# Optimization experiments

Hardware: AMD Instinct MI355X
Metric: run time of the kernel (lower is better)

Reference implementation:

```python
import jax, jax.numpy as jnp
import numpy as np

B, S, D, H, G = 16, 512, 1024, 128, 256  # batch, seq, lstm_in, lstm_hidden, gat_dim

def _linear(x, W, b):
    return x @ W.T + b

def _lstm_dir(xs, Wih, Whh, bih, bhh, reverse):
    # xs: [S, B, Din] -> hs: [S, B, H]; PyTorch gate order i, f, g, o
    b = bih + bhh
    def step(carry, xt):
        h, c = carry
        z = xt @ Wih.T + h @ Whh.T + b
        i, f, g, o = jnp.split(z, 4, axis=-1)
        c = jax.nn.sigmoid(f) * c + jax.nn.sigmoid(i) * jnp.tanh(g)
        h = jax.nn.sigmoid(o) * jnp.tanh(c)
        return (h, c), h
    init = (jnp.zeros((xs.shape[1], Whh.shape[1]), xs.dtype),
            jnp.zeros((xs.shape[1], Whh.shape[1]), xs.dtype))
    _, hs = jax.lax.scan(step, init, xs, reverse=reverse)
    return hs

def _forward(x, adj,
             l0f_Wih, l0f_Whh, l0f_bih, l0f_bhh, l0b_Wih, l0b_Whh, l0b_bih, l0b_bhh,
             l1f_Wih, l1f_Whh, l1f_bih, l1f_bhh, l1b_Wih, l1b_Whh, l1b_bih, l1b_bhh,
             fc1_W, fc1_b, wattn_W, wattn_b, lin0_W, lin0_b, lin1_W, lin1_b,
             linf_W, linf_b, fcA_W, fcA_b, fcB_W, fcB_b, fcC_W, fcC_b):
    # ---- 2-layer bidirectional LSTM ----
    xs = jnp.swapaxes(x, 0, 1)  # [S, B, D]
    h0 = jnp.concatenate([_lstm_dir(xs, l0f_Wih, l0f_Whh, l0f_bih, l0f_bhh, False),
                          _lstm_dir(xs, l0b_Wih, l0b_Whh, l0b_bih, l0b_bhh, True)], axis=-1)
    h1 = jnp.concatenate([_lstm_dir(h0, l1f_Wih, l1f_Whh, l1f_bih, l1f_bhh, False),
                          _lstm_dir(h0, l1b_Wih, l1b_Whh, l1b_bih, l1b_bhh, True)], axis=-1)
    out_lstm = jnp.swapaxes(h1, 0, 1)  # [B, S, 2H]
    # ---- GAT on fc1(x) ----
    g = _linear(x, fc1_W, fc1_b)  # [B, S, G]
    idx = jnp.arange(S)
    adj = adj.at[:, idx, idx].set(1.0)
    eye = 1e-05 * jnp.eye(S, dtype=x.dtype)
    for l in range(4):
        g0 = g
        q = _linear(g, wattn_W[l], wattn_b[l])
        a = jax.nn.sigmoid(jnp.einsum('bij,bkj->bik', q, g)) + eye
        a = a * adj
        a = a / jnp.sum(a, axis=2, keepdims=True)
        g = jnp.einsum('bij,bjd->bid', a, g)
        g = jax.nn.relu(_linear(g, lin0_W[l], lin0_b[l]))
        g = jax.nn.relu(_linear(g, lin1_W[l], lin1_b[l]))
        g = g + g0
    g = _linear(g, linf_W, linf_b)
    # ---- head (dropout in eval mode -> identity) ----
    hidden = jnp.mean(jnp.concatenate([out_lstm, g], axis=2), axis=1)  # [B, 512]
    y = jax.nn.leaky_relu(_linear(hidden, fcA_W, fcA_b), 0.1)
    y = jax.nn.leaky_relu(_linear(y, fcB_W, fcB_b), 0.1)
    y = _linear(y, fcC_W, fcC_b)  # [B, 2]
    return y, hidden


def setup_inputs() -> dict:
    key = jax.random.key(0)
    ks = jax.random.split(key, 40)
    r = lambda k, shape: jax.random.normal(k, shape, jnp.float32) * 0.05
    inp = {}
    inp['x'] = jax.random.normal(ks[0], (B, S, D), jnp.float32)
    inp['adj'] = (jax.random.uniform(ks[1], (B, S, S)) < 0.05).astype(jnp.float32)
    # LSTM params: layer0 input D, layer1 input 2H; forward/backward directions
    inp['l0f_Wih'] = r(ks[2], (4 * H, D)); inp['l0f_Whh'] = r(ks[3], (4 * H, H))
    inp['l0f_bih'] = r(ks[4], (4 * H,));  inp['l0f_bhh'] = r(ks[5], (4 * H,))
    inp['l0b_Wih'] = r(ks[6], (4 * H, D)); inp['l0b_Whh'] = r(ks[7], (4 * H, H))
    inp['l0b_bih'] = r(ks[8], (4 * H,));  inp['l0b_bhh'] = r(ks[9], (4 * H,))
    inp['l1f_Wih'] = r(ks[10], (4 * H, 2 * H)); inp['l1f_Whh'] = r(ks[11], (4 * H, H))
    inp['l1f_bih'] = r(ks[12], (4 * H,)); inp['l1f_bhh'] = r(ks[13], (4 * H,))
    inp['l1b_Wih'] = r(ks[14], (4 * H, 2 * H)); inp['l1b_Whh'] = r(ks[15], (4 * H, H))
    inp['l1b_bih'] = r(ks[16], (4 * H,)); inp['l1b_bhh'] = r(ks[17], (4 * H,))
    inp['fc1_W'] = r(ks[18], (G, D)); inp['fc1_b'] = r(ks[19], (G,))
    inp['wattn_W'] = r(ks[20], (4, G, G)); inp['wattn_b'] = r(ks[21], (4, G))
    inp['lin0_W'] = r(ks[22], (4, G, G)); inp['lin0_b'] = r(ks[23], (4, G))
    inp['lin1_W'] = r(ks[24], (4, G, G)); inp['lin1_b'] = r(ks[25], (4, G))
    inp['linf_W'] = r(ks[26], (G, G)); inp['linf_b'] = r(ks[27], (G,))
    inp['fcA_W'] = r(ks[28], (128, 512)); inp['fcA_b'] = r(ks[29], (128,))
    inp['fcB_W'] = r(ks[30], (32, 128)); inp['fcB_b'] = r(ks[31], (32,))
    inp['fcC_W'] = r(ks[32], (2, 32)); inp['fcC_b'] = r(ks[33], (2,))
    return inp


def reference(x, adj,
              l0f_Wih, l0f_Whh, l0f_bih, l0f_bhh, l0b_Wih, l0b_Whh, l0b_bih, l0b_bhh,
              l1f_Wih, l1f_Whh, l1f_bih, l1f_bhh, l1b_Wih, l1b_Whh, l1b_bih, l1b_bhh,
              fc1_W, fc1_b, wattn_W, wattn_b, lin0_W, lin0_b, lin1_W, lin1_b,
              linf_W, linf_b, fcA_W, fcA_b, fcB_W, fcB_b, fcC_W, fcC_b):
    return _forward(x, adj,
                    l0f_Wih, l0f_Whh, l0f_bih, l0f_bhh, l0b_Wih, l0b_Whh, l0b_bih, l0b_bhh,
                    l1f_Wih, l1f_Whh, l1f_bih, l1f_bhh, l1b_Wih, l1b_Whh, l1b_bih, l1b_bhh,
                    fc1_W, fc1_b, wattn_W, wattn_b, lin0_W, lin0_b, lin1_W, lin1_b,
                    linf_W, linf_b, fcA_W, fcA_b, fcB_W, fcB_b, fcC_W, fcC_b)
```

## Files before the change

### kernel.cpp

```cpp
#include <hip/hip_runtime.h>
#include <stdint.h>

#define B_ 16
#define S_ 512
#define D_ 1024
#define H4 512
#define G_ 256

typedef unsigned short u16;
using short8 = __attribute__((ext_vector_type(8))) short;
using f32x4  = __attribute__((ext_vector_type(4))) float;

__device__ __forceinline__ u16 f2bf(float f){
  unsigned int u = __float_as_uint(f);
  u += 0x7fffu + ((u >> 16) & 1u);
  return (u16)(u >> 16);
}
__device__ __forceinline__ float bf2f(u16 h){
  return __uint_as_float(((unsigned int)h) << 16);
}

struct CvtSegs {
  const float4* src[14];
  short4* dst[14];
  int blk0[15];
};
__global__ __launch_bounds__(256) void cvt_multi(CvtSegs cs){
  int blk = blockIdx.x;
  int s = 0;
  #pragma unroll
  for (int k = 0; k < 14; ++k) if (cs.blk0[k + 1] <= blk) s = k + 1;
  int i = (blk - cs.blk0[s]) * 256 + threadIdx.x;
  float4 v = cs.src[s][i];
  short4 o;
  o.x = (short)f2bf(v.x); o.y = (short)f2bf(v.y);
  o.z = (short)f2bf(v.z); o.w = (short)f2bf(v.w);
  cs.dst[s][i] = o;
}

__global__ __launch_bounds__(256) void bias_prep(const float* a,const float* b,const float* c,const float* d,
                                                 const float* e,const float* f,const float* g,const float* h,
                                                 float* out){
  int i = blockIdx.x * 256 + threadIdx.x;
  if (i >= 2048) return;
  int p = i >> 9, k = i & 511;
  const float* x1 = (p==0)?a:(p==1)?c:(p==2)?e:g;
  const float* x2 = (p==0)?b:(p==1)?d:(p==2)?f:h;
  out[i] = x1[k] + x2[k];
}

template<int ACT, bool OUT_BF16, int PERM, bool RESID>
__device__ __forceinline__ void gemm_bt_body(
    const u16* __restrict__ A, const u16* __restrict__ W,
    const float* __restrict__ bias, const u16* __restrict__ resid,
    void* __restrict__ outp, int M, int N, int K,
    long sA, long sW, long sO, int bx, int by, int bz)
{
  const u16* Ab = A + (long)bz * sA;
  const u16* Wb = W + (long)bz * sW;
  const int bm0 = by * 64, bn0 = bx * 64;
  const int tid = threadIdx.x;
  const int l = tid & 63, wid = tid >> 6;
  const int wm = (wid >> 1) * 32, wn = (wid & 1) * 32;
  const int lr = l & 15, lk8 = (l >> 4) * 8;

  const f32x4 z4 = {0.f, 0.f, 0.f, 0.f};
  f32x4 acc[2][2] = {{z4, z4}, {z4, z4}};

  const u16* Ap0 = Ab + (long)(bm0 + wm + lr) * K + lk8;
  const u16* Wp0 = Wb + (long)(bn0 + wn + lr) * K + lk8;
  for (int k0 = 0; k0 < K; k0 += 32) {
    short8 a0 = *reinterpret_cast<const short8*>(Ap0 + k0);
    short8 a1 = *reinterpret_cast<const short8*>(Ap0 + (long)16 * K + k0);
    short8 b0 = *reinterpret_cast<const short8*>(Wp0 + k0);
    short8 b1 = *reinterpret_cast<const short8*>(Wp0 + (long)16 * K + k0);
    acc[0][0] = __builtin_amdgcn_mfma_f32_16x16x32_bf16(a0, b0, acc[0][0], 0, 0, 0);
    acc[0][1] = __builtin_amdgcn_mfma_f32_16x16x32_bf16(a0, b1, acc[0][1], 0, 0, 0);
    acc[1][0] = __builtin_amdgcn_mfma_f32_16x16x32_bf16(a1, b0, acc[1][0], 0, 0, 0);
    acc[1][1] = __builtin_amdgcn_mfma_f32_16x16x32_bf16(a1, b1, acc[1][1], 0, 0, 0);
  }
  #pragma unroll
  for (int mt = 0; mt < 2; ++mt)
  #pragma unroll
  for (int nt = 0; nt < 2; ++nt) {
    int n = bn0 + wn + 16 * nt + lr;
    float bv = bias ? bias[n] : 0.f;
    #pragma unroll
    for (int r = 0; r < 4; ++r) {
      int m = bm0 + wm + 16 * mt + (l >> 4) * 4 + r;
      float v = acc[mt][nt][r] + bv;
      if (ACT == 1) v = fmaxf(v, 0.f);
      if (RESID) v += bf2f(resid[(long)m * N + n]);
      long oi;
      if (PERM == 2) {
        int t = m & 511, b = m >> 9;
        oi = (long)((t * 16 + b) * 128 + (n & 127)) * 4 + (n >> 7);
      } else {
        oi = (long)bz * sO + (long)m * N + n;
      }
      if (OUT_BF16) ((u16*)outp)[oi] = f2bf(v);
      else          ((float*)outp)[oi] = v;
    }
  }
}

template<int ACT, bool OUT_BF16, int PERM, bool RESID>
__global__ __launch_bounds__(256) void gemm_bt(
    const u16* __restrict__ A, const u16* __restrict__ W,
    const float* __restrict__ bias, const u16* __restrict__ resid,
    void* __restrict__ outp, int M, int N, int K,
    long sA, long sW, long sO)
{
  gemm_bt_body<ACT, OUT_BF16, PERM, RESID>(A, W, bias, resid, outp, M, N, K,
                                           sA, sW, sO, blockIdx.x, blockIdx.y, blockIdx.z);
}

__device__ __forceinline__ void lstm_scan_body(
    const float* __restrict__ X, const u16* __restrict__ Whh,
    u16* __restrict__ Hout, int dir, int bg)
{
  __shared__ __align__(16) u16 h_lds[16 * 136];
  __shared__ float z_lds[4 * 516];

  const int tid = threadIdx.x;
  const int l = tid & 63, w = tid >> 6;
  const int lr = l & 15, lk = l >> 4;

  short8 bfrag[4][4];
  #pragma unroll
  for (int nt = 0; nt < 4; ++nt)
    #pragma unroll
    for (int ks = 0; ks < 4; ++ks)
      bfrag[nt][ks] = *reinterpret_cast<const short8*>(
          Whh + (64 * w + 16 * nt + lr) * 128 + 32 * ks + 8 * lk);

  for (int i = tid; i < 16 * 136; i += 512) h_lds[i] = 0;

  const int j  = tid & 127;
  const int bq = tid >> 7;
  float c = 0.f;
  const f32x4 z4 = {0.f, 0.f, 0.f, 0.f};

  __syncthreads();

  auto ldX = [&](int t) -> float4 {
    int ta = dir ? (S_ - 1 - t) : t;
    return *reinterpret_cast<const float4*>(X + (long)((ta * 16 + bg + bq) * 128 + j) * 4);
  };

  float4 x0 = ldX(0), x1 = ldX(1), x2 = ldX(2), x3;

  auto step = [&](int t, float4& xc, float4& xt, int tload) {
    short8 af[4];
    #pragma unroll
    for (int ks = 0; ks < 4; ++ks)
      af[ks] = *reinterpret_cast<const short8*>(h_lds + lr * 136 + 32 * ks + 8 * lk);
    f32x4 acc[4] = {z4, z4, z4, z4};
    #pragma unroll
    for (int nt = 0; nt < 4; ++nt)
      #pragma unroll
      for (int ks = 0; ks < 4; ++ks)
        acc[nt] = __builtin_amdgcn_mfma_f32_16x16x32_bf16(af[ks], bfrag[nt][ks], acc[nt], 0, 0, 0);
    if (lk == 0) {
      #pragma unroll
      for (int nt = 0; nt < 4; ++nt)
        #pragma unroll
        for (int r = 0; r < 4; ++r)
          z_lds[r * 516 + 64 * w + 16 * nt + lr] = acc[nt][r];
    }
    if (tload < S_) xt = ldX(tload);
    asm volatile("s_waitcnt lgkmcnt(0)" ::: "memory");
    __builtin_amdgcn_s_barrier();
    int ta = dir ? (S_ - 1 - t) : t;
    float zi = z_lds[bq * 516 + j      ] + xc.x;
    float zf = z_lds[bq * 516 + 128 + j] + xc.y;
    float zg = z_lds[bq * 516 + 256 + j] + xc.z;
    float zo = z_lds[bq * 516 + 384 + j] + xc.w;
    float si = __fdividef(1.f, 1.f + __expf(-zi));
    float sf = __fdividef(1.f, 1.f + __expf(-zf));
    float so = __fdividef(1.f, 1.f + __expf(-zo));
    float eg = __expf(2.f * zg);
    float tg = 1.f - __fdividef(2.f, eg + 1.f);
    c = sf * c + si * tg;
    float ec = __expf(2.f * c);
    float tc = 1.f - __fdividef(2.f, ec + 1.f);
    float hv = so * tc;
    u16 hb = f2bf(hv);
    h_lds[bq * 136 + j] = hb;
    Hout[((long)(bg + bq) * S_ + ta) * 256 + dir * 128 + j] = hb;
    asm volatile("s_waitcnt lgkmcnt(0)" ::: "memory");
    __builtin_amdgcn_s_barrier();
  };

  for (int t = 0; t < S_; t += 4) {
    step(t,     x0, x3, t + 3);
    step(t + 1, x1, x0, t + 4);
    step(t + 2, x2, x1, t + 5);
    step(t + 3, x3, x2, t + 6);
  }
}

__global__ __launch_bounds__(512, 1) void scan_fused(
    const float* __restrict__ Xf, const float* __restrict__ Xb,
    const u16* __restrict__ Whhf, const u16* __restrict__ Whhb,
    u16* __restrict__ Hout,
    const u16* __restrict__ gA, const u16* __restrict__ gW,
    const float* __restrict__ gb, u16* __restrict__ gOut, int gK)
{
  if (blockIdx.x < 8) {
    int dir = blockIdx.x & 1, bg = (blockIdx.x >> 1) * 4;
    lstm_scan_body(dir ? Xb : Xf, dir ? Whhb : Whhf, Hout, dir, bg);
  } else if (threadIdx.x < 256) {
    int bi = blockIdx.x - 8;
    gemm_bt_body<0, true, 0, false>(gA, gW, gb, nullptr, gOut,
                                    8192, 256, gK, 0, 0, 0, bi & 3, bi >> 2, 0);
  }
}

__global__ __launch_bounds__(256) void attn_norm(
    const float* __restrict__ sc, const float* __restrict__ adj, u16* __restrict__ abf)
{
  int bz = blockIdx.y;
  int i = blockIdx.x * 4 + (threadIdx.x >> 6);
  int l = threadIdx.x & 63;
  const float* srow = sc  + ((long)bz * 512 + i) * 512;
  const float* arow = adj + ((long)bz * 512 + i) * 512;
  float av[8]; float sum = 0.f;
  #pragma unroll
  for (int k = 0; k < 8; ++k) {
    int jj = l + 64 * k;
    float sg = __fdividef(1.f, 1.f + __expf(-srow[jj]));
    float v = (jj == i) ? (sg + 1e-5f) : sg * arow[jj];
    av[k] = v; sum += v;
  }
  #pragma unroll
  for (int off = 32; off; off >>= 1) sum += __shfl_xor(sum, off);
  float r = __fdividef(1.f, sum);
  u16* orow = abf + ((long)bz * 512 + i) * 512;
  #pragma unroll
  for (int k = 0; k < 8; ++k) orow[l + 64 * k] = f2bf(av[k] * r);
}

__global__ __launch_bounds__(256) void transpose_g(const u16* __restrict__ in, u16* __restrict__ out)
{
  __shared__ u16 tile[32][33];
  int bz = blockIdx.z;
  int s0 = blockIdx.x * 32, d0 = blockIdx.y * 32;
  int tx = threadIdx.x & 31, ty = threadIdx.x >> 5;
  const u16* ip = in + (long)bz * 512 * 256;
  u16* op = out + (long)bz * 256 * 512;
  #pragma unroll
  for (int k = 0; k < 32; k += 8) tile[ty + k][tx] = ip[(long)(s0 + ty + k) * 256 + d0 + tx];
  __syncthreads();
  #pragma unroll
  for (int k = 0; k < 32; k += 8) op[(long)(d0 + ty + k) * 512 + s0 + tx] = tile[tx][ty + k];
}

__global__ __launch_bounds__(256) void mean_cat(
    const u16* __restrict__ lstm, const u16* __restrict__ gf, float* __restrict__ dout)
{
  int b = blockIdx.x;
  for (int cc = threadIdx.x; cc < 512; cc += 256) {
    const u16* src = (cc < 256) ? (lstm + (long)b * 512 * 256 + cc)
                                : (gf   + (long)b * 512 * 256 + (cc - 256));
    float s = 0.f;
    for (int t = 0; t < 512; ++t) s += bf2f(src[(long)t * 256]);
    dout[32 + b * 512 + cc] = s * (1.f / 512.f);
  }
}

__global__ __launch_bounds__(256) void head_kernel(
    const float* __restrict__ hidden,
    const float* __restrict__ fcA_W, const float* __restrict__ fcA_b,
    const float* __restrict__ fcB_W, const float* __restrict__ fcB_b,
    const float* __restrict__ fcC_W, const float* __restrict__ fcC_b,
    float* __restrict__ y)
{
  __shared__ float hb[16 * 512];
  __shared__ float ab[16 * 128];
  __shared__ float bb[16 * 32];
  int tid = threadIdx.x;
  for (int i = tid; i < 8192; i += 256) hb[i] = hidden[i];
  __syncthreads();
  for (int o = tid; o < 2048; o += 256) {
    int b = o >> 7, jj = o & 127;
    float acc = fcA_b[jj];
    const float* wrow = fcA_W + jj * 512;
    const float* hrow = hb + b * 512;
    for (int k = 0; k < 512; ++k) acc += hrow[k] * wrow[k];
    ab[o] = acc > 0.f ? acc : 0.1f * acc;
  }
  __syncthreads();
  for (int o = tid; o < 512; o += 256) {
    int b = o >> 5, jj = o & 31;
    float acc = fcB_b[jj];
    for (int k = 0; k < 128; ++k) acc += ab[b * 128 + k] * fcB_W[jj * 128 + k];
    bb[o] = acc > 0.f ? acc : 0.1f * acc;
  }
  __syncthreads();
  if (tid < 32) {
    int b = tid >> 1, jj = tid & 1;
    float acc = fcC_b[jj];
    for (int k = 0; k < 32; ++k) acc += bb[b * 32 + k] * fcC_W[jj * 32 + k];
    y[b * 2 + jj] = acc;
  }
}

extern "C" void kernel_launch(void* const* d_in, const int* in_sizes, int n_in,
                              void* d_out, int out_size, void* d_ws, size_t ws_size,
                              hipStream_t stream)
{
  const float* x       = (const float*)d_in[0];
  const float* adj     = (const float*)d_in[1];
  const float* l0f_Wih = (const float*)d_in[2];
  const float* l0f_Whh = (const float*)d_in[3];
  const float* l0f_bih = (const float*)d_in[4];
  const float* l0f_bhh = (const float*)d_in[5];
  const float* l0b_Wih = (const float*)d_in[6];
  const float* l0b_Whh = (const float*)d_in[7];
  const float* l0b_bih = (const float*)d_in[8];
  const float* l0b_bhh = (const float*)d_in[9];
  const float* l1f_Wih = (const float*)d_in[10];
  const float* l1f_Whh = (const float*)d_in[11];
  const float* l1f_bih = (const float*)d_in[12];
  const float* l1f_bhh = (const float*)d_in[13];
  const float* l1b_Wih = (const float*)d_in[14];
  const float* l1b_Whh = (const float*)d_in[15];
  const float* l1b_bih = (const float*)d_in[16];
  const float* l1b_bhh = (const float*)d_in[17];
  const float* fc1_W   = (const float*)d_in[18];
  const float* fc1_b   = (const float*)d_in[19];
  const float* wattn_W = (const float*)d_in[20];
  const float* wattn_b = (const float*)d_in[21];
  const float* lin0_W  = (const float*)d_in[22];
  const float* lin0_b  = (const float*)d_in[23];
  const float* lin1_W  = (const float*)d_in[24];
  const float* lin1_b  = (const float*)d_in[25];
  const float* linf_W  = (const float*)d_in[26];
  const float* linf_b  = (const float*)d_in[27];
  const float* fcA_W   = (const float*)d_in[28];
  const float* fcA_b   = (const float*)d_in[29];
  const float* fcB_W   = (const float*)d_in[30];
  const float* fcB_b   = (const float*)d_in[31];
  const float* fcC_W   = (const float*)d_in[32];
  const float* fcC_b   = (const float*)d_in[33];

  char* wp = (char*)d_ws;
  auto alloc = [&](size_t n) -> void* { void* p = wp; wp += (n + 255) & ~(size_t)255; return p; };

  u16* x_bf     = (u16*)alloc((size_t)B_ * S_ * D_ * 2);
  u16* w0f_ih   = (u16*)alloc((size_t)512 * 1024 * 2);
  u16* w0f_hh   = (u16*)alloc((size_t)512 * 128 * 2);
  u16* w0b_ih   = (u16*)alloc((size_t)512 * 1024 * 2);
  u16* w0b_hh   = (u16*)alloc((size_t)512 * 128 * 2);
  u16* w1f_ih   = (u16*)alloc((size_t)512 * 256 * 2);
  u16* w1f_hh   = (u16*)alloc((size_t)512 * 128 * 2);
  u16* w1b_ih   = (u16*)alloc((size_t)512 * 256 * 2);
  u16* w1b_hh   = (u16*)alloc((size_t)512 * 128 * 2);
  u16* wfc1     = (u16*)alloc((size_t)256 * 1024 * 2);
  u16* wattn_bf = (u16*)alloc((size_t)4 * 256 * 256 * 2);
  u16* wlin0_bf = (u16*)alloc((size_t)4 * 256 * 256 * 2);
  u16* wlin1_bf = (u16*)alloc((size_t)4 * 256 * 256 * 2);
  u16* wlinf_bf = (u16*)alloc((size_t)256 * 256 * 2);
  float* bias4  = (float*)alloc((size_t)2048 * 4);
  float* X0f    = (float*)alloc((size_t)S_ * 16 * 512 * 4);
  float* X0b    = (float*)alloc((size_t)S_ * 16 * 512 * 4);
  u16* h0       = (u16*)alloc((size_t)B_ * S_ * 256 * 2);
  u16* lstm_out = (u16*)alloc((size_t)B_ * S_ * 256 * 2);
  u16* gA       = (u16*)alloc((size_t)B_ * S_ * 256 * 2);
  u16* gB       = (u16*)alloc((size_t)B_ * S_ * 256 * 2);
  u16* qb       = (u16*)alloc((size_t)B_ * S_ * 256 * 2);
  u16* gT       = (u16*)alloc((size_t)B_ * S_ * 256 * 2);
  u16* t1       = (u16*)alloc((size_t)B_ * S_ * 256 * 2);
  u16* t2       = (u16*)alloc((size_t)B_ * S_ * 256 * 2);
  float* sc     = (float*)alloc((size_t)B_ * S_ * S_ * 4);
  u16* abf      = (u16*)alloc((size_t)B_ * S_ * S_ * 2);

  CvtSegs cs;
  int nb = 0, si = 0;
  auto seg = [&](const float* s, u16* d, int n) {
    cs.src[si] = (const float4*)s; cs.dst[si] = (short4*)d;
    cs.blk0[si] = nb; nb += (n / 4 + 255) / 256; ++si;
  };
  seg(x, x_bf, B_ * S_ * D_);
  seg(l0f_Wih, w0f_ih, 512 * 1024); seg(l0f_Whh, w0f_hh, 512 * 128);
  seg(l0b_Wih, w0b_ih, 512 * 1024); seg(l0b_Whh, w0b_hh, 512 * 128);
  seg(l1f_Wih, w1f_ih, 512 * 256);  seg(l1f_Whh, w1f_hh, 512 * 128);
  seg(l1b_Wih, w1b_ih, 512 * 256);  seg(l1b_Whh, w1b_hh, 512 * 128);
  seg(fc1_W, wfc1, 256 * 1024);
  seg(wattn_W, wattn_bf, 4 * 256 * 256);
  seg(lin0_W, wlin0_bf, 4 * 256 * 256);
  seg(lin1_W, wlin1_bf, 4 * 256 * 256);
  seg(linf_W, wlinf_bf, 256 * 256);
  cs.blk0[si] = nb;
  cvt_multi<<<nb, 256, 0, stream>>>(cs);
  bias_prep<<<8, 256, 0, stream>>>(l0f_bih, l0f_bhh, l0b_bih, l0b_bhh,
                                   l1f_bih, l1f_bhh, l1b_bih, l1b_bhh, bias4);

  gemm_bt<0, false, 2, false><<<dim3(8, 128, 1), 256, 0, stream>>>(
      x_bf, w0f_ih, bias4 + 0, nullptr, X0f, 8192, 512, 1024, 0, 0, 0);
  gemm_bt<0, false, 2, false><<<dim3(8, 128, 1), 256, 0, stream>>>(
      x_bf, w0b_ih, bias4 + 512, nullptr, X0b, 8192, 512, 1024, 0, 0, 0);
  scan_fused<<<8 + 512, 512, 0, stream>>>(X0f, X0b, w0f_hh, w0b_hh, h0,
                                          x_bf, wfc1, fc1_b, gA, 1024);
  gemm_bt<0, false, 2, false><<<dim3(8, 128, 1), 256, 0, stream>>>(
      h0, w1f_ih, bias4 + 1024, nullptr, X0f, 8192, 512, 256, 0, 0, 0);
  gemm_bt<0, false, 2, false><<<dim3(8, 128, 1), 256, 0, stream>>>(
      h0, w1b_ih, bias4 + 1536, nullptr, X0b, 8192, 512, 256, 0, 0, 0);
  scan_fused<<<8 + 512, 512, 0, stream>>>(X0f, X0b, w1f_hh, w1b_hh, lstm_out,
                                          gA, wattn_bf, wattn_b, qb, 256);

  u16* gcur = gA; u16* gnext = gB;
  for (int lyr = 0; lyr < 4; ++lyr) {
    if (lyr > 0)
      gemm_bt<0, true, 0, false><<<dim3(4, 128, 1), 256, 0, stream>>>(
          gcur, wattn_bf + lyr * 65536, wattn_b + lyr * 256, nullptr, qb, 8192, 256, 256, 0, 0, 0);
    gemm_bt<0, false, 0, false><<<dim3(8, 8, 16), 256, 0, stream>>>(
        qb, gcur, nullptr, nullptr, sc, 512, 512, 256, 131072, 131072, 262144);
    attn_norm<<<dim3(128, 16), 256, 0, stream>>>(sc, adj, abf);
    transpose_g<<<dim3(16, 8, 16), 256, 0, stream>>>(gcur, gT);
    gemm_bt<0, true, 0, false><<<dim3(4, 8, 16), 256, 0, stream>>>(
        abf, gT, nullptr, nullptr, t1, 512, 256, 512, 262144, 131072, 131072);
    gemm_bt<1, true, 0, false><<<dim3(4, 128, 1), 256, 0, stream>>>(
        t1, wlin0_bf + lyr * 65536, lin0_b + lyr * 256, nullptr, t2, 8192, 256, 256, 0, 0, 0);
    gemm_bt<1, true, 0, true><<<dim3(4, 128, 1), 256, 0, stream>>>(
        t2, wlin1_bf + lyr * 65536, lin1_b + lyr * 256, gcur, gnext, 8192, 256, 256, 0, 0, 0);
    u16* tmp = gcur; gcur = gnext; gnext = tmp;
  }
  gemm_bt<0, true, 0, false><<<dim3(4, 128, 1), 256, 0, stream>>>(
      gcur, wlinf_bf, linf_b, nullptr, t2, 8192, 256, 256, 0, 0, 0);

  mean_cat<<<16, 256, 0, stream>>>(lstm_out, t2, (float*)d_out);
  head_kernel<<<1, 256, 0, stream>>>((const float*)d_out + 32,
                                     fcA_W, fcA_b, fcB_W, fcB_b, fcC_W, fcC_b,
                                     (float*)d_out);
}
```

Before: 1.506 ms.

## Interleave two batch chains per LSTM scan block with gate-interleaved weights

The LSTM recurrence now runs 4 blocks instead of 8, and each block advances two independent 4-batch chains. The chains are interleaved so one chain's MFMA work overlaps the other's gate math. W_hh rows are permuted into gate-interleaved order and the MFMA operands are swapped, so each lane gets its i,f,g,o pre-activations for one unit as a single vector. A double-buffered h buffer lets each timestep end with one barrier instead of two. In exchange, each block does twice the serial work per step, and fewer blocks run the scan.

```diff
diff --git a/kernel.cpp b/kernel.cpp
--- a/kernel.cpp
+++ b/kernel.cpp
@@ -36,6 +36,21 @@
   o.x = (short)f2bf(v.x); o.y = (short)f2bf(v.y);
   o.z = (short)f2bf(v.z); o.w = (short)f2bf(v.w);
   cs.dst[s][i] = o;
+}
+
+__global__ __launch_bounds__(256) void cvt_whh(const float* m0, const float* m1,
+                                               const float* m2, const float* m3,
+                                               u16* out){
+  int e = blockIdx.x * 256 + threadIdx.x;
+  int row = e >> 4;
+  int kk = (e & 15) * 8;
+  int mat = row >> 9, c = row & 511;
+  const float* src = (mat == 0 ? m0 : mat == 1 ? m1 : mat == 2 ? m2 : m3)
+                     + ((c & 3) * 128 + (c >> 2)) * 128 + kk;
+  u16* dst = out + (size_t)row * 128 + kk;
+  float4 v0 = *(const float4*)src, v1 = *(const float4*)(src + 4);
+  dst[0] = f2bf(v0.x); dst[1] = f2bf(v0.y); dst[2] = f2bf(v0.z); dst[3] = f2bf(v0.w);
+  dst[4] = f2bf(v1.x); dst[5] = f2bf(v1.y); dst[6] = f2bf(v1.z); dst[7] = f2bf(v1.w);
 }
 
 __global__ __launch_bounds__(256) void bias_prep(const float* a,const float* b,const float* c,const float* d,
@@ -115,103 +130,109 @@
                                            sA, sW, sO, blockIdx.x, blockIdx.y, blockIdx.z);
 }
 
-__device__ __forceinline__ void lstm_scan_body(
-    const float* __restrict__ X, const u16* __restrict__ Whh,
-    u16* __restrict__ Hout, int dir, int bg)
-{
-  __shared__ __align__(16) u16 h_lds[16 * 136];
-  __shared__ float z_lds[4 * 516];
+__device__ __forceinline__ void lstm_scan2_body(
+    const float* __restrict__ X, const u16* __restrict__ Wp,
+    u16* __restrict__ Hout, int dir, int batA, int batB)
+{
+  __shared__ __align__(16) u16 hbuf[2][2][16][4][8];
+  __shared__ __align__(16) float zq[2][8][16][4][4];
 
   const int tid = threadIdx.x;
   const int l = tid & 63, w = tid >> 6;
   const int lr = l & 15, lk = l >> 4;
-
-  short8 bfrag[4][4];
+  const int j = 16 * w + lr;
+
+  short8 wfrag[4][4];
   #pragma unroll
   for (int nt = 0; nt < 4; ++nt)
     #pragma unroll
     for (int ks = 0; ks < 4; ++ks)
-      bfrag[nt][ks] = *reinterpret_cast<const short8*>(
-          Whh + (64 * w + 16 * nt + lr) * 128 + 32 * ks + 8 * lk);
-
-  for (int i = tid; i < 16 * 136; i += 512) h_lds[i] = 0;
-
-  const int j  = tid & 127;
-  const int bq = tid >> 7;
-  float c = 0.f;
+      wfrag[nt][ks] = *reinterpret_cast<const short8*>(
+          Wp + (64 * w + 16 * nt + lr) * 128 + 32 * ks + 8 * lk);
+
+  for (int i = tid; i < (int)(sizeof(hbuf) / 2); i += 512) ((u16*)hbuf)[i] = 0;
+
+  float cA = 0.f, cB = 0.f;
+
+  auto ldX = [&](int bat, int t) -> float4 {
+    int ta = dir ? (S_ - 1 - t) : t;
+    return *reinterpret_cast<const float4*>(X + (size_t)((ta * 16 + bat + lk) * 128 + j) * 4);
+  };
+
+  float4 a0 = ldX(batA, 0), a1 = ldX(batA, 1), a2 = ldX(batA, 2), a3;
+  float4 b0 = ldX(batB, 0), b1 = ldX(batB, 1), b2 = ldX(batB, 2), b3;
+
+  __syncthreads();
+
   const f32x4 z4 = {0.f, 0.f, 0.f, 0.f};
 
-  __syncthreads();
-
-  auto ldX = [&](int t) -> float4 {
-    int ta = dir ? (S_ - 1 - t) : t;
-    return *reinterpret_cast<const float4*>(X + (long)((ta * 16 + bg + bq) * 128 + j) * 4);
-  };
-
-  float4 x0 = ldX(0), x1 = ldX(1), x2 = ldX(2), x3;
-
-  auto step = [&](int t, float4& xc, float4& xt, int tload) {
-    short8 af[4];
+  auto mfma_half = [&](int ch, int p) {
+    short8 hf[4];
     #pragma unroll
     for (int ks = 0; ks < 4; ++ks)
-      af[ks] = *reinterpret_cast<const short8*>(h_lds + lr * 136 + 32 * ks + 8 * lk);
+      hf[ks] = *reinterpret_cast<const short8*>(&hbuf[ch][p][lk + 4 * ks][lr & 3][0]);
     f32x4 acc[4] = {z4, z4, z4, z4};
     #pragma unroll
     for (int nt = 0; nt < 4; ++nt)
       #pragma unroll
       for (int ks = 0; ks < 4; ++ks)
-        acc[nt] = __builtin_amdgcn_mfma_f32_16x16x32_bf16(af[ks], bfrag[nt][ks], acc[nt], 0, 0, 0);
-    if (lk == 0) {
+        acc[nt] = __builtin_amdgcn_mfma_f32_16x16x32_bf16(wfrag[nt][ks], hf[ks], acc[nt], 0, 0, 0);
+    if (lr < 4) {
       #pragma unroll
       for (int nt = 0; nt < 4; ++nt)
-        #pragma unroll
-        for (int r = 0; r < 4; ++r)
-          z_lds[r * 516 + 64 * w + 16 * nt + lr] = acc[nt][r];
+        *reinterpret_cast<f32x4*>(&zq[ch][w][4 * nt + lk][lr][0]) = acc[nt];
     }
-    if (tload < S_) xt = ldX(tload);
-    asm volatile("s_waitcnt lgkmcnt(0)" ::: "memory");
-    __builtin_amdgcn_s_barrier();
-    int ta = dir ? (S_ - 1 - t) : t;
-    float zi = z_lds[bq * 516 + j      ] + xc.x;
-    float zf = z_lds[bq * 516 + 128 + j] + xc.y;
-    float zg = z_lds[bq * 516 + 256 + j] + xc.z;
-    float zo = z_lds[bq * 516 + 384 + j] + xc.w;
+  };
+
+  auto gates = [&](int ch, float& cs, const float4& xc, int bat, int t, int p) {
+    f32x4 q = *reinterpret_cast<const f32x4*>(&zq[ch][w][lr][lk][0]);
+    float zi = q[0] + xc.x, zf = q[1] + xc.y, zg = q[2] + xc.z, zo = q[3] + xc.w;
     float si = __fdividef(1.f, 1.f + __expf(-zi));
     float sf = __fdividef(1.f, 1.f + __expf(-zf));
     float so = __fdividef(1.f, 1.f + __expf(-zo));
     float eg = __expf(2.f * zg);
     float tg = 1.f - __fdividef(2.f, eg + 1.f);
-    c = sf * c + si * tg;
-    float ec = __expf(2.f * c);
+    cs = sf * cs + si * tg;
+    float ec = __expf(2.f * cs);
     float tc = 1.f - __fdividef(2.f, ec + 1.f);
     float hv = so * tc;
     u16 hb = f2bf(hv);
-    h_lds[bq * 136 + j] = hb;
-    Hout[((long)(bg + bq) * S_ + ta) * 256 + dir * 128 + j] = hb;
+    hbuf[ch][p ^ 1][j >> 3][lk][j & 7] = hb;
+    int ta = dir ? (S_ - 1 - t) : t;
+    Hout[((size_t)(bat + lk) * S_ + ta) * 256 + dir * 128 + j] = hb;
+  };
+
+  auto period = [&](int t, float4& xA, float4& xB, float4& pA, float4& pB, int tload) {
+    const int p = t & 1;
+    mfma_half(0, p);
+    mfma_half(1, p);
+    gates(0, cA, xA, batA, t, p);
+    gates(1, cB, xB, batB, t, p);
+    if (tload < S_) { pA = ldX(batA, tload); pB = ldX(batB, tload); }
     asm volatile("s_waitcnt lgkmcnt(0)" ::: "memory");
     __builtin_amdgcn_s_barrier();
   };
 
   for (int t = 0; t < S_; t += 4) {
-    step(t,     x0, x3, t + 3);
-    step(t + 1, x1, x0, t + 4);
-    step(t + 2, x2, x1, t + 5);
-    step(t + 3, x3, x2, t + 6);
+    period(t,     a0, b0, a3, b3, t + 3);
+    period(t + 1, a1, b1, a0, b0, t + 4);
+    period(t + 2, a2, b2, a1, b1, t + 5);
+    period(t + 3, a3, b3, a2, b2, t + 6);
   }
 }
 
 __global__ __launch_bounds__(512, 1) void scan_fused(
     const float* __restrict__ Xf, const float* __restrict__ Xb,
-    const u16* __restrict__ Whhf, const u16* __restrict__ Whhb,
+    const u16* __restrict__ WpF, const u16* __restrict__ WpB,
     u16* __restrict__ Hout,
     const u16* __restrict__ gA, const u16* __restrict__ gW,
     const float* __restrict__ gb, u16* __restrict__ gOut, int gK)
 {
-  if (blockIdx.x < 8) {
-    int dir = blockIdx.x & 1, bg = (blockIdx.x >> 1) * 4;
-    lstm_scan_body(dir ? Xb : Xf, dir ? Whhb : Whhf, Hout, dir, bg);
+  if (blockIdx.x < 4) {
+    int dir = blockIdx.x >> 1, pr = blockIdx.x & 1;
+    lstm_scan2_body(dir ? Xb : Xf, dir ? WpB : WpF, Hout, dir, pr * 8, pr * 8 + 4);
   } else if (threadIdx.x < 256) {
-    int bi = blockIdx.x - 8;
+    int bi = blockIdx.x - 4;
     gemm_bt_body<0, true, 0, false>(gA, gW, gb, nullptr, gOut,
                                     8192, 256, gK, 0, 0, 0, bi & 3, bi >> 2, 0);
   }
@@ -350,13 +371,10 @@
 
   u16* x_bf     = (u16*)alloc((size_t)B_ * S_ * D_ * 2);
   u16* w0f_ih   = (u16*)alloc((size_t)512 * 1024 * 2);
-  u16* w0f_hh   = (u16*)alloc((size_t)512 * 128 * 2);
   u16* w0b_ih   = (u16*)alloc((size_t)512 * 1024 * 2);
-  u16* w0b_hh   = (u16*)alloc((size_t)512 * 128 * 2);
   u16* w1f_ih   = (u16*)alloc((size_t)512 * 256 * 2);
-  u16* w1f_hh   = (u16*)alloc((size_t)512 * 128 * 2);
   u16* w1b_ih   = (u16*)alloc((size_t)512 * 256 * 2);
-  u16* w1b_hh   = (u16*)alloc((size_t)512 * 128 * 2);
+  u16* wI       = (u16*)alloc((size_t)4 * 512 * 128 * 2);
   u16* wfc1     = (u16*)alloc((size_t)256 * 1024 * 2);
   u16* wattn_bf = (u16*)alloc((size_t)4 * 256 * 256 * 2);
   u16* wlin0_bf = (u16*)alloc((size_t)4 * 256 * 256 * 2);
@@ -383,17 +401,18 @@
     cs.blk0[si] = nb; nb += (n / 4 + 255) / 256; ++si;
   };
   seg(x, x_bf, B_ * S_ * D_);
-  seg(l0f_Wih, w0f_ih, 512 * 1024); seg(l0f_Whh, w0f_hh, 512 * 128);
-  seg(l0b_Wih, w0b_ih, 512 * 1024); seg(l0b_Whh, w0b_hh, 512 * 128);
-  seg(l1f_Wih, w1f_ih, 512 * 256);  seg(l1f_Whh, w1f_hh, 512 * 128);
-  seg(l1b_Wih, w1b_ih, 512 * 256);  seg(l1b_Whh, w1b_hh, 512 * 128);
+  seg(l0f_Wih, w0f_ih, 512 * 1024);
+  seg(l0b_Wih, w0b_ih, 512 * 1024);
+  seg(l1f_Wih, w1f_ih, 512 * 256);
+  seg(l1b_Wih, w1b_ih, 512 * 256);
   seg(fc1_W, wfc1, 256 * 1024);
   seg(wattn_W, wattn_bf, 4 * 256 * 256);
   seg(lin0_W, wlin0_bf, 4 * 256 * 256);
   seg(lin1_W, wlin1_bf, 4 * 256 * 256);
   seg(linf_W, wlinf_bf, 256 * 256);
-  cs.blk0[si] = nb;
+  for (int k = si; k <= 14; ++k) cs.blk0[k] = nb;
   cvt_multi<<<nb, 256, 0, stream>>>(cs);
+  cvt_whh<<<128, 256, 0, stream>>>(l0f_Whh, l0b_Whh, l1f_Whh, l1b_Whh, wI);
   bias_prep<<<8, 256, 0, stream>>>(l0f_bih, l0f_bhh, l0b_bih, l0b_bhh,
                                    l1f_bih, l1f_bhh, l1b_bih, l1b_bhh, bias4);
 
@@ -401,13 +420,13 @@
       x_bf, w0f_ih, bias4 + 0, nullptr, X0f, 8192, 512, 1024, 0, 0, 0);
   gemm_bt<0, false, 2, false><<<dim3(8, 128, 1), 256, 0, stream>>>(
       x_bf, w0b_ih, bias4 + 512, nullptr, X0b, 8192, 512, 1024, 0, 0, 0);
-  scan_fused<<<8 + 512, 512, 0, stream>>>(X0f, X0b, w0f_hh, w0b_hh, h0,
+  scan_fused<<<4 + 512, 512, 0, stream>>>(X0f, X0b, wI + 0 * 65536, wI + 1 * 65536, h0,
                                           x_bf, wfc1, fc1_b, gA, 1024);
   gemm_bt<0, false, 2, false><<<dim3(8, 128, 1), 256, 0, stream>>>(
       h0, w1f_ih, bias4 + 1024, nullptr, X0f, 8192, 512, 256, 0, 0, 0);
   gemm_bt<0, false, 2, false><<<dim3(8, 128, 1), 256, 0, stream>>>(
       h0, w1b_ih, bias4 + 1536, nullptr, X0b, 8192, 512, 256, 0, 0, 0);
-  scan_fused<<<8 + 512, 512, 0, stream>>>(X0f, X0b, w1f_hh, w1b_hh, lstm_out,
+  scan_fused<<<4 + 512, 512, 0, stream>>>(X0f, X0b, wI + 2 * 65536, wI + 3 * 65536, lstm_out,
                                           gA, wattn_bf, wattn_b, qb, 256);
 
   u16* gcur = gA; u16* gnext = gB;
```

Result: slower. 2.102 ms (+39.6%).

## Split LSTM scan into 16 blocks of two batches and use direct-load side GEMM

Applied to the files above, without the earlier changes.

The recurrent scan now runs on 16 workgroups, each handling two batch rows instead of four, which halves the per-step gate work and the z_lds traffic per block. MFMA work per step is unchanged because the 16-row tile is padded, so only the half of threads with bq<2 compute gates. The side GEMM fused into the same launch is replaced by a simpler 64x128 tile kernel that loads operands straight from global memory without LDS staging, and it uses all 512 threads across 256 blocks. Weight conversion segments are reordered, which has no speed intent. The trade-off is twice as many serial-latency scan blocks and a GEMM with less data reuse.

```diff
diff --git a/kernel.cpp b/kernel.cpp
--- a/kernel.cpp
+++ b/kernel.cpp
@@ -115,12 +115,52 @@
                                            sA, sW, sO, blockIdx.x, blockIdx.y, blockIdx.z);
 }
 
-__device__ __forceinline__ void lstm_scan_body(
+__device__ __forceinline__ void gemm_bt_body8(
+    const u16* __restrict__ A, const u16* __restrict__ W,
+    const float* __restrict__ bias, u16* __restrict__ out,
+    int N, int K, int bx, int by)
+{
+  const int bm0 = by * 64, bn0 = bx * 128;
+  const int tid = threadIdx.x;
+  const int l = tid & 63, wid = tid >> 6;
+  const int wm = (wid >> 2) * 32, wn = (wid & 3) * 32;
+  const int lr = l & 15, lk8 = (l >> 4) * 8;
+
+  const f32x4 z4 = {0.f, 0.f, 0.f, 0.f};
+  f32x4 acc[2][2] = {{z4, z4}, {z4, z4}};
+
+  const u16* Ap0 = A + (long)(bm0 + wm + lr) * K + lk8;
+  const u16* Wp0 = W + (long)(bn0 + wn + lr) * K + lk8;
+  for (int k0 = 0; k0 < K; k0 += 32) {
+    short8 a0 = *reinterpret_cast<const short8*>(Ap0 + k0);
+    short8 a1 = *reinterpret_cast<const short8*>(Ap0 + (long)16 * K + k0);
+    short8 b0 = *reinterpret_cast<const short8*>(Wp0 + k0);
+    short8 b1 = *reinterpret_cast<const short8*>(Wp0 + (long)16 * K + k0);
+    acc[0][0] = __builtin_amdgcn_mfma_f32_16x16x32_bf16(a0, b0, acc[0][0], 0, 0, 0);
+    acc[0][1] = __builtin_amdgcn_mfma_f32_16x16x32_bf16(a0, b1, acc[0][1], 0, 0, 0);
+    acc[1][0] = __builtin_amdgcn_mfma_f32_16x16x32_bf16(a1, b0, acc[1][0], 0, 0, 0);
+    acc[1][1] = __builtin_amdgcn_mfma_f32_16x16x32_bf16(a1, b1, acc[1][1], 0, 0, 0);
+  }
+  #pragma unroll
+  for (int mt = 0; mt < 2; ++mt)
+  #pragma unroll
+  for (int nt = 0; nt < 2; ++nt) {
+    int n = bn0 + wn + 16 * nt + lr;
+    float bv = bias[n];
+    #pragma unroll
+    for (int r = 0; r < 4; ++r) {
+      int m = bm0 + wm + 16 * mt + (l >> 4) * 4 + r;
+      out[(long)m * N + n] = f2bf(acc[mt][nt][r] + bv);
+    }
+  }
+}
+
+__device__ __forceinline__ void lstm_scan7_body(
     const float* __restrict__ X, const u16* __restrict__ Whh,
     u16* __restrict__ Hout, int dir, int bg)
 {
   __shared__ __align__(16) u16 h_lds[16 * 136];
-  __shared__ float z_lds[4 * 516];
+  __shared__ float z_lds[2 * 516];
 
   const int tid = threadIdx.x;
   const int l = tid & 63, w = tid >> 6;
@@ -139,16 +179,17 @@
   const int j  = tid & 127;
   const int bq = tid >> 7;
   float c = 0.f;
+  float4 xA, xB, xC, xD;
+
+  __syncthreads();
+
+  auto loadX = [&](int t) -> float4 {
+    int ta = dir ? (S_ - 1 - t) : t;
+    return *reinterpret_cast<const float4*>(X + (size_t)((ta * 16 + bg + bq) * 128 + j) * 4);
+  };
+  if (bq < 2) { xA = loadX(0); xB = loadX(1); xC = loadX(2); }
+
   const f32x4 z4 = {0.f, 0.f, 0.f, 0.f};
-
-  __syncthreads();
-
-  auto ldX = [&](int t) -> float4 {
-    int ta = dir ? (S_ - 1 - t) : t;
-    return *reinterpret_cast<const float4*>(X + (long)((ta * 16 + bg + bq) * 128 + j) * 4);
-  };
-
-  float4 x0 = ldX(0), x1 = ldX(1), x2 = ldX(2), x3;
 
   auto step = [&](int t, float4& xc, float4& xt, int tload) {
     short8 af[4];
@@ -165,38 +206,40 @@
       #pragma unroll
       for (int nt = 0; nt < 4; ++nt)
         #pragma unroll
-        for (int r = 0; r < 4; ++r)
+        for (int r = 0; r < 2; ++r)
           z_lds[r * 516 + 64 * w + 16 * nt + lr] = acc[nt][r];
     }
-    if (tload < S_) xt = ldX(tload);
+    if (bq < 2 && tload < S_) xt = loadX(tload);
     asm volatile("s_waitcnt lgkmcnt(0)" ::: "memory");
     __builtin_amdgcn_s_barrier();
-    int ta = dir ? (S_ - 1 - t) : t;
-    float zi = z_lds[bq * 516 + j      ] + xc.x;
-    float zf = z_lds[bq * 516 + 128 + j] + xc.y;
-    float zg = z_lds[bq * 516 + 256 + j] + xc.z;
-    float zo = z_lds[bq * 516 + 384 + j] + xc.w;
-    float si = __fdividef(1.f, 1.f + __expf(-zi));
-    float sf = __fdividef(1.f, 1.f + __expf(-zf));
-    float so = __fdividef(1.f, 1.f + __expf(-zo));
-    float eg = __expf(2.f * zg);
-    float tg = 1.f - __fdividef(2.f, eg + 1.f);
-    c = sf * c + si * tg;
-    float ec = __expf(2.f * c);
-    float tc = 1.f - __fdividef(2.f, ec + 1.f);
-    float hv = so * tc;
-    u16 hb = f2bf(hv);
-    h_lds[bq * 136 + j] = hb;
-    Hout[((long)(bg + bq) * S_ + ta) * 256 + dir * 128 + j] = hb;
+    if (bq < 2) {
+      int ta = dir ? (S_ - 1 - t) : t;
+      float zi = z_lds[bq * 516 + j      ] + xc.x;
+      float zf = z_lds[bq * 516 + 128 + j] + xc.y;
+      float zg = z_lds[bq * 516 + 256 + j] + xc.z;
+      float zo = z_lds[bq * 516 + 384 + j] + xc.w;
+      float si = __fdividef(1.f, 1.f + __expf(-zi));
+      float sf = __fdividef(1.f, 1.f + __expf(-zf));
+      float so = __fdividef(1.f, 1.f + __expf(-zo));
+      float eg = __expf(2.f * zg);
+      float tg = 1.f - __fdividef(2.f, eg + 1.f);
+      c = sf * c + si * tg;
+      float ec = __expf(2.f * c);
+      float tc = 1.f - __fdividef(2.f, ec + 1.f);
+      float hv = so * tc;
+      u16 hb = f2bf(hv);
+      h_lds[bq * 136 + j] = hb;
+      Hout[((size_t)(bg + bq) * S_ + ta) * 256 + dir * 128 + j] = hb;
+    }
     asm volatile("s_waitcnt lgkmcnt(0)" ::: "memory");
     __builtin_amdgcn_s_barrier();
   };
 
   for (int t = 0; t < S_; t += 4) {
-    step(t,     x0, x3, t + 3);
-    step(t + 1, x1, x0, t + 4);
-    step(t + 2, x2, x1, t + 5);
-    step(t + 3, x3, x2, t + 6);
+    step(t,     xA, xD, t + 3);
+    step(t + 1, xB, xA, t + 4);
+    step(t + 2, xC, xB, t + 5);
+    step(t + 3, xD, xC, t + 6);
   }
 }
 
@@ -207,13 +250,12 @@
     const u16* __restrict__ gA, const u16* __restrict__ gW,
     const float* __restrict__ gb, u16* __restrict__ gOut, int gK)
 {
-  if (blockIdx.x < 8) {
-    int dir = blockIdx.x & 1, bg = (blockIdx.x >> 1) * 4;
-    lstm_scan_body(dir ? Xb : Xf, dir ? Whhb : Whhf, Hout, dir, bg);
-  } else if (threadIdx.x < 256) {
-    int bi = blockIdx.x - 8;
-    gemm_bt_body<0, true, 0, false>(gA, gW, gb, nullptr, gOut,
-                                    8192, 256, gK, 0, 0, 0, bi & 3, bi >> 2, 0);
+  if (blockIdx.x < 16) {
+    int dir = blockIdx.x & 1, bg = (blockIdx.x >> 1) * 2;
+    lstm_scan7_body(dir ? Xb : Xf, dir ? Whhb : Whhf, Hout, dir, bg);
+  } else {
+    int bi = blockIdx.x - 16;
+    gemm_bt_body8(gA, gW, gb, gOut, 256, gK, bi & 1, bi >> 1);
   }
 }
 
@@ -350,12 +392,12 @@
 
   u16* x_bf     = (u16*)alloc((size_t)B_ * S_ * D_ * 2);
   u16* w0f_ih   = (u16*)alloc((size_t)512 * 1024 * 2);
+  u16* w0b_ih   = (u16*)alloc((size_t)512 * 1024 * 2);
+  u16* w1f_ih   = (u16*)alloc((size_t)512 * 256 * 2);
+  u16* w1b_ih   = (u16*)alloc((size_t)512 * 256 * 2);
   u16* w0f_hh   = (u16*)alloc((size_t)512 * 128 * 2);
-  u16* w0b_ih   = (u16*)alloc((size_t)512 * 1024 * 2);
   u16* w0b_hh   = (u16*)alloc((size_t)512 * 128 * 2);
-  u16* w1f_ih   = (u16*)alloc((size_t)512 * 256 * 2);
   u16* w1f_hh   = (u16*)alloc((size_t)512 * 128 * 2);
-  u16* w1b_ih   = (u16*)alloc((size_t)512 * 256 * 2);
   u16* w1b_hh   = (u16*)alloc((size_t)512 * 128 * 2);
   u16* wfc1     = (u16*)alloc((size_t)256 * 1024 * 2);
   u16* wattn_bf = (u16*)alloc((size_t)4 * 256 * 256 * 2);
@@ -383,16 +425,20 @@
     cs.blk0[si] = nb; nb += (n / 4 + 255) / 256; ++si;
   };
   seg(x, x_bf, B_ * S_ * D_);
-  seg(l0f_Wih, w0f_ih, 512 * 1024); seg(l0f_Whh, w0f_hh, 512 * 128);
-  seg(l0b_Wih, w0b_ih, 512 * 1024); seg(l0b_Whh, w0b_hh, 512 * 128);
-  seg(l1f_Wih, w1f_ih, 512 * 256);  seg(l1f_Whh, w1f_hh, 512 * 128);
-  seg(l1b_Wih, w1b_ih, 512 * 256);  seg(l1b_Whh, w1b_hh, 512 * 128);
+  seg(l0f_Wih, w0f_ih, 512 * 1024);
+  seg(l0b_Wih, w0b_ih, 512 * 1024);
+  seg(l1f_Wih, w1f_ih, 512 * 256);
+  seg(l1b_Wih, w1b_ih, 512 * 256);
+  seg(l0f_Whh, w0f_hh, 512 * 128);
+  seg(l0b_Whh, w0b_hh, 512 * 128);
+  seg(l1f_Whh, w1f_hh, 512 * 128);
+  seg(l1b_Whh, w1b_hh, 512 * 128);
   seg(fc1_W, wfc1, 256 * 1024);
   seg(wattn_W, wattn_bf, 4 * 256 * 256);
   seg(lin0_W, wlin0_bf, 4 * 256 * 256);
   seg(lin1_W, wlin1_bf, 4 * 256 * 256);
   seg(linf_W, wlinf_bf, 256 * 256);
-  cs.blk0[si] = nb;
+  for (int k = si; k <= 14; ++k) cs.blk0[k] = nb;
   cvt_multi<<<nb, 256, 0, stream>>>(cs);
   bias_prep<<<8, 256, 0, stream>>>(l0f_bih, l0f_bhh, l0b_bih, l0b_bhh,
                                    l1f_bih, l1f_bhh, l1b_bih, l1b_bhh, bias4);
@@ -401,14 +447,14 @@
       x_bf, w0f_ih, bias4 + 0, nullptr, X0f, 8192, 512, 1024, 0, 0, 0);
   gemm_bt<0, false, 2, false><<<dim3(8, 128, 1), 256, 0, stream>>>(
       x_bf, w0b_ih, bias4 + 512, nullptr, X0b, 8192, 512, 1024, 0, 0, 0);
-  scan_fused<<<8 + 512, 512, 0, stream>>>(X0f, X0b, w0f_hh, w0b_hh, h0,
-                                          x_bf, wfc1, fc1_b, gA, 1024);
+  scan_fused<<<16 + 256, 512, 0, stream>>>(X0f, X0b, w0f_hh, w0b_hh, h0,
+                                           x_bf, wfc1, fc1_b, gA, 1024);
   gemm_bt<0, false, 2, false><<<dim3(8, 128, 1), 256, 0, stream>>>(
       h0, w1f_ih, bias4 + 1024, nullptr, X0f, 8192, 512, 256, 0, 0, 0);
   gemm_bt<0, false, 2, false><<<dim3(8, 128, 1), 256, 0, stream>>>(
       h0, w1b_ih, bias4 + 1536, nullptr, X0b, 8192, 512, 256, 0, 0, 0);
-  scan_fused<<<8 + 512, 512, 0, stream>>>(X0f, X0b, w1f_hh, w1b_hh, lstm_out,
-                                          gA, wattn_bf, wattn_b, qb, 256);
+  scan_fused<<<16 + 256, 512, 0, stream>>>(X0f, X0b, w1f_hh, w1b_hh, lstm_out,
+                                           gA, wattn_bf, wattn_b, qb, 256);
 
   u16* gcur = gA; u16* gnext = gB;
   for (int lyr = 0; lyr < 4; ++lyr) {
```

After: 1.360 ms. 9.7% less time.
